# Kernel optimization log

Measured on AMD Instinct MI355X. Metric: run time of the kernel, lower is better.

## Reference

```python
import jax, jax.numpy as jnp
import numpy as np

N_NODES = 100000
N_EDGES = 800000
D_NODE = 64
D_EDGE = 16
D_OUT = 64
D_ATT = 2 * D_OUT + D_EDGE  # 144


def setup_inputs() -> dict:
    key = jax.random.key(0)
    ks = jax.random.split(key, 10)
    node_features = jax.random.normal(ks[0], (N_NODES, D_NODE), dtype=jnp.float32)
    edge_node_indices = jax.random.randint(ks[1], (2, N_EDGES), 0, N_NODES, dtype=jnp.int64)
    edge_features = jax.random.normal(ks[2], (N_EDGES, D_EDGE), dtype=jnp.float32)
    # Linear weights (torch convention: W is [out, in]); uniform(size, w) style init approximated
    def uni(k, shape, size):
        bound = 1.0 / np.sqrt(size)
        return jax.random.uniform(k, shape, dtype=jnp.float32, minval=-bound, maxval=bound)
    W_n = uni(ks[3], (D_OUT, D_NODE), D_NODE)
    b_n = uni(ks[4], (D_OUT,), D_NODE)
    W_e = uni(ks[5], (D_EDGE, D_EDGE), D_EDGE)
    b_e = uni(ks[6], (D_EDGE,), D_EDGE)
    W_a = uni(ks[7], (1, D_ATT), D_ATT)
    b_a = uni(ks[8], (1,), D_ATT)
    return {
        "node_features": node_features,
        "edge_node_indices": edge_node_indices,
        "edge_features": edge_features,
        "W_n": W_n, "b_n": b_n,
        "W_e": W_e, "b_e": b_e,
        "W_a": W_a, "b_a": b_a,
    }


def reference(node_features, edge_node_indices, edge_features, W_n, b_n, W_e, b_e, W_a, b_a):
    node0_idx = edge_node_indices[0]
    node1_idx = edge_node_indices[1]
    n_nodes = node_features.shape[0]

    # gather + linear projections  [E, D_OUT] / [E, D_EDGE]
    node0_out = node_features[node0_idx] @ W_n.T + b_n
    node1_out = node_features[node1_idx] @ W_n.T + b_n
    edge_out = edge_features @ W_e.T + b_e

    # attention over concat -> scalar per edge  [E, 1]
    att_in = jnp.concatenate([node0_out, node1_out, edge_out], axis=1)
    att_out = att_in @ W_a.T + b_a
    # faithful to original: softmax along dim=1 of an [E,1] tensor (== all ones)
    attention = jax.nn.softmax(jax.nn.leaky_relu(att_out, negative_slope=0.01), axis=1)

    # attenuate and scatter-sum back to nodes
    attenuated = attention * node0_out  # [E, D_OUT]
    z = jax.ops.segment_sum(attenuated, node0_idx, num_segments=n_nodes)
    return z
```

## Files before the change

### kernel.cpp

```cpp
#include <hip/hip_runtime.h>
#include <hip/hip_bf16.h>

#define N_NODES 100000
#define N_EDGES 800000
#define D 64
#define SLICES 64
#define QUARTERS 4
#define HIST_BLOCKS (SLICES * QUARTERS)
#define NQUART 25000
#define HWORDS_Q 6272
#define QUADS (N_EDGES / 4)
#define QPS (QUADS / SLICES)
#define XPAD 72

typedef __attribute__((ext_vector_type(8))) short bf16x8;
typedef __attribute__((ext_vector_type(4))) float f32x4;


__global__ __launch_bounds__(1024) void hist_kernel(
        const int* __restrict__ idx32,
        unsigned*  __restrict__ part) {
    __shared__ __align__(16) unsigned h[HWORDS_Q];
    uint4* __restrict__ h4 = (uint4*)h;
    for (int i = threadIdx.x; i < HWORDS_Q / 4; i += 1024)
        h4[i] = uint4{0u, 0u, 0u, 0u};

    const int lane = threadIdx.x & 63;
    int s = 0;
#pragma unroll
    for (int k = 0; k < 4; ++k) s |= idx32[2 * (lane + 64 * k) + 1];
    const bool is64 = (__ballot(s != 0) == 0ULL);

    __syncthreads();

    const int slice = blockIdx.x >> 2;
    const int q     = blockIdx.x & 3;
    const int base  = q * NQUART;

    for (int t = slice * QPS + threadIdx.x; t < (slice + 1) * QPS; t += 1024) {
        int v[4];
        if (is64) {
            const int4 a = ((const int4*)idx32)[2 * t + 0];
            const int4 b = ((const int4*)idx32)[2 * t + 1];
            v[0] = a.x; v[1] = a.z; v[2] = b.x; v[3] = b.z;
        } else {
            const int4 a = ((const int4*)idx32)[t];
            v[0] = a.x; v[1] = a.y; v[2] = a.z; v[3] = a.w;
        }
#pragma unroll
        for (int j = 0; j < 4; ++j) {
            const unsigned u = (unsigned)(v[j] - base);
            if (u < (unsigned)NQUART)
                atomicAdd(&h[u >> 2], 1u << (8 * (u & 3)));
        }
    }

    __syncthreads();

    uint4* __restrict__ dst = (uint4*)(part + (size_t)blockIdx.x * HWORDS_Q);
    for (int i = threadIdx.x; i < HWORDS_Q / 4; i += 1024) dst[i] = h4[i];
}

__device__ inline unsigned bf16rn(float f) {
    const unsigned u = __float_as_uint(f);
    return (u + 0x7FFFu + ((u >> 16) & 1u)) >> 16;
}
__device__ inline unsigned pk2(float lo, float hi) {
    return bf16rn(lo) | (bf16rn(hi) << 16);
}

__global__ __launch_bounds__(256, 4) void proj_kernel(
        const float* __restrict__ nf,
        const float* __restrict__ Wn,
        const float* __restrict__ bn,
        const unsigned* __restrict__ part,
        float* __restrict__ out) {
    __shared__ __align__(16) unsigned short xs[64 * XPAD];
    __shared__ __align__(16) unsigned short wl[64 * XPAD];
    __shared__ unsigned cnt_p[4][64];

    const int t = threadIdx.x;
    const int base = blockIdx.x * 64;
    const int lane = t & 63;
    const int wv = __builtin_amdgcn_readfirstlane(t >> 6);

    {
        const int r = t >> 2;
        const int c0 = (t & 3) * 16;
        const float* __restrict__ src = Wn + r * D + c0;
        const float4 v0 = *reinterpret_cast<const float4*>(src + 0);
        const float4 v1 = *reinterpret_cast<const float4*>(src + 4);
        const float4 v2 = *reinterpret_cast<const float4*>(src + 8);
        const float4 v3 = *reinterpret_cast<const float4*>(src + 12);
        uint4 lo, hi;
        lo.x = pk2(v0.x, v0.y); lo.y = pk2(v0.z, v0.w);
        lo.z = pk2(v1.x, v1.y); lo.w = pk2(v1.z, v1.w);
        hi.x = pk2(v2.x, v2.y); hi.y = pk2(v2.z, v2.w);
        hi.z = pk2(v3.x, v3.y); hi.w = pk2(v3.z, v3.w);
        *reinterpret_cast<uint4*>(&wl[r * XPAD + c0 + 0]) = lo;
        *reinterpret_cast<uint4*>(&wl[r * XPAD + c0 + 8]) = hi;
    }

    {
        const int r = t >> 2;
        const int c0 = (t & 3) * 16;
        const int node = min(base + r, N_NODES - 1);
        const float* __restrict__ src = nf + (size_t)node * D + c0;
        const float4 v0 = *reinterpret_cast<const float4*>(src + 0);
        const float4 v1 = *reinterpret_cast<const float4*>(src + 4);
        const float4 v2 = *reinterpret_cast<const float4*>(src + 8);
        const float4 v3 = *reinterpret_cast<const float4*>(src + 12);
        uint4 lo, hi;
        lo.x = pk2(v0.x, v0.y); lo.y = pk2(v0.z, v0.w);
        lo.z = pk2(v1.x, v1.y); lo.w = pk2(v1.z, v1.w);
        hi.x = pk2(v2.x, v2.y); hi.y = pk2(v2.z, v2.w);
        hi.z = pk2(v3.x, v3.y); hi.w = pk2(v3.z, v3.w);
        *reinterpret_cast<uint4*>(&xs[r * XPAD + c0 + 0]) = lo;
        *reinterpret_cast<uint4*>(&xs[r * XPAD + c0 + 8]) = hi;
    }

    {
        const int node = min(base + lane, N_NODES - 1);
        const int q = node / NQUART;
        const int lw = (node - q * NQUART) >> 2;
        const int sh = 8 * (node & 3);
        unsigned s = 0;
#pragma unroll
        for (int k = 0; k < 16; ++k) {
            const int b = 16 * wv + k;
            s += (part[(size_t)(4 * b + q) * HWORDS_Q + lw] >> sh) & 255u;
        }
        cnt_p[wv][lane] = s;
    }

    __syncthreads();

    const int l15 = lane & 15;
    const int lhi = lane >> 4;

    const unsigned short* __restrict__ arow = &xs[(wv * 16 + l15) * XPAD + lhi * 8];
    const bf16x8 a0 = *reinterpret_cast<const bf16x8*>(arow + 0);
    const bf16x8 a1 = *reinterpret_cast<const bf16x8*>(arow + 32);

    f32x4 acc[4];
#pragma unroll
    for (int nt = 0; nt < 4; ++nt) {
        const float b = bn[nt * 16 + l15];
        acc[nt] = f32x4{b, b, b, b};
    }

#pragma unroll
    for (int nt = 0; nt < 4; ++nt) {
        const unsigned short* __restrict__ brow =
            &wl[(nt * 16 + l15) * XPAD + lhi * 8];
        const bf16x8 b0 = *reinterpret_cast<const bf16x8*>(brow + 0);
        const bf16x8 b1 = *reinterpret_cast<const bf16x8*>(brow + 32);
        acc[nt] = __builtin_amdgcn_mfma_f32_16x16x32_bf16(a0, b0, acc[nt], 0, 0, 0);
        acc[nt] = __builtin_amdgcn_mfma_f32_16x16x32_bf16(a1, b1, acc[nt], 0, 0, 0);
    }

    float cf[4];
#pragma unroll
    for (int r = 0; r < 4; ++r) {
        const int m = wv * 16 + lhi * 4 + r;
        cf[r] = (float)(cnt_p[0][m] + cnt_p[1][m] + cnt_p[2][m] + cnt_p[3][m]);
    }

#pragma unroll
    for (int nt = 0; nt < 4; ++nt) {
#pragma unroll
        for (int r = 0; r < 4; ++r) {
            const int node = base + wv * 16 + lhi * 4 + r;
            if (node < N_NODES)
                out[(size_t)node * D + nt * 16 + l15] = cf[r] * acc[nt][r];
        }
    }
}

extern "C" void kernel_launch(void* const* d_in, const int* in_sizes, int n_in,
                              void* d_out, int out_size, void* d_ws, size_t ws_size,
                              hipStream_t stream) {
    const float* nf   = (const float*)d_in[0];
    const int*   eidx = (const int*)d_in[1];
    const float* Wn   = (const float*)d_in[3];
    const float* bn   = (const float*)d_in[4];
    float* out = (float*)d_out;

    unsigned* part = (unsigned*)d_ws;

    hist_kernel<<<HIST_BLOCKS, 1024, 0, stream>>>(eidx, part);

    proj_kernel<<<(N_NODES + 63) / 64, 256, 0, stream>>>(
        nf, Wn, bn, part, out);
}
```

Before: 24.41 us.

## Fuse histogram and projection into one cooperative kernel with grid sync

Merges the per-node edge-count histogram kernel and the bf16 MFMA projection kernel into a single cooperative launch of 256 blocks of 1024 threads, separated by a grid-wide barrier. The projection phase becomes a persistent loop over 256-node tiles, reusing the converted weight tile and bias across tiles. The aim is to remove the second launch and the gap between kernels. In exchange it adds grid-sync overhead, runs fewer threads in the projection phase than the many small blocks did before, and relies on cooperative launch residency.

Result: slower. 67.65 us (+177.2%).

```diff
diff --git a/kernel.cpp b/kernel.cpp
--- a/kernel.cpp
+++ b/kernel.cpp
@@ -1,65 +1,26 @@
 #include <hip/hip_runtime.h>
 #include <hip/hip_bf16.h>
+#include <hip/hip_cooperative_groups.h>
+
+namespace cg = cooperative_groups;
 
 #define N_NODES 100000
 #define N_EDGES 800000
 #define D 64
 #define SLICES 64
 #define QUARTERS 4
-#define HIST_BLOCKS (SLICES * QUARTERS)
 #define NQUART 25000
 #define HWORDS_Q 6272
 #define QUADS (N_EDGES / 4)
 #define QPS (QUADS / SLICES)
 #define XPAD 72
+#define TILE 256
+#define N_TILES ((N_NODES + TILE - 1) / TILE)
+#define GRID 256
 
 typedef __attribute__((ext_vector_type(8))) short bf16x8;
 typedef __attribute__((ext_vector_type(4))) float f32x4;
 
-
-__global__ __launch_bounds__(1024) void hist_kernel(
-        const int* __restrict__ idx32,
-        unsigned*  __restrict__ part) {
-    __shared__ __align__(16) unsigned h[HWORDS_Q];
-    uint4* __restrict__ h4 = (uint4*)h;
-    for (int i = threadIdx.x; i < HWORDS_Q / 4; i += 1024)
-        h4[i] = uint4{0u, 0u, 0u, 0u};
-
-    const int lane = threadIdx.x & 63;
-    int s = 0;
-#pragma unroll
-    for (int k = 0; k < 4; ++k) s |= idx32[2 * (lane + 64 * k) + 1];
-    const bool is64 = (__ballot(s != 0) == 0ULL);
-
-    __syncthreads();
-
-    const int slice = blockIdx.x >> 2;
-    const int q     = blockIdx.x & 3;
-    const int base  = q * NQUART;
-
-    for (int t = slice * QPS + threadIdx.x; t < (slice + 1) * QPS; t += 1024) {
-        int v[4];
-        if (is64) {
-            const int4 a = ((const int4*)idx32)[2 * t + 0];
-            const int4 b = ((const int4*)idx32)[2 * t + 1];
-            v[0] = a.x; v[1] = a.z; v[2] = b.x; v[3] = b.z;
-        } else {
-            const int4 a = ((const int4*)idx32)[t];
-            v[0] = a.x; v[1] = a.y; v[2] = a.z; v[3] = a.w;
-        }
-#pragma unroll
-        for (int j = 0; j < 4; ++j) {
-            const unsigned u = (unsigned)(v[j] - base);
-            if (u < (unsigned)NQUART)
-                atomicAdd(&h[u >> 2], 1u << (8 * (u & 3)));
-        }
-    }
-
-    __syncthreads();
-
-    uint4* __restrict__ dst = (uint4*)(part + (size_t)blockIdx.x * HWORDS_Q);
-    for (int i = threadIdx.x; i < HWORDS_Q / 4; i += 1024) dst[i] = h4[i];
-}
 
 __device__ inline unsigned bf16rn(float f) {
     const unsigned u = __float_as_uint(f);
@@ -69,22 +30,73 @@
     return bf16rn(lo) | (bf16rn(hi) << 16);
 }
 
-__global__ __launch_bounds__(256, 4) void proj_kernel(
+#define SMEM_BYTES 50176
+
+__global__ __launch_bounds__(1024, 2) void fused_kernel(
+        const int*   __restrict__ idx32,
         const float* __restrict__ nf,
         const float* __restrict__ Wn,
         const float* __restrict__ bn,
-        const unsigned* __restrict__ part,
-        float* __restrict__ out) {
-    __shared__ __align__(16) unsigned short xs[64 * XPAD];
-    __shared__ __align__(16) unsigned short wl[64 * XPAD];
-    __shared__ unsigned cnt_p[4][64];
-
+        unsigned*    __restrict__ part,
+        float*       __restrict__ out) {
+    __shared__ __align__(16) unsigned char smem[SMEM_BYTES];
     const int t = threadIdx.x;
-    const int base = blockIdx.x * 64;
     const int lane = t & 63;
+    cg::grid_group grid = cg::this_grid();
+
+    {
+        unsigned* __restrict__ h = (unsigned*)smem;
+        uint4* __restrict__ h4 = (uint4*)smem;
+        for (int i = t; i < HWORDS_Q / 4; i += 1024)
+            h4[i] = uint4{0u, 0u, 0u, 0u};
+
+        int s = 0;
+#pragma unroll
+        for (int k = 0; k < 4; ++k) s |= idx32[2 * (lane + 64 * k) + 1];
+        const bool is64 = (__ballot(s != 0) == 0ULL);
+
+        __syncthreads();
+
+        const int slice = blockIdx.x >> 2;
+        const int q     = blockIdx.x & 3;
+        const int base  = q * NQUART;
+
+        for (int tq = slice * QPS + t; tq < (slice + 1) * QPS; tq += 1024) {
+            int v[4];
+            if (is64) {
+                const int4 a = ((const int4*)idx32)[2 * tq + 0];
+                const int4 b = ((const int4*)idx32)[2 * tq + 1];
+                v[0] = a.x; v[1] = a.z; v[2] = b.x; v[3] = b.z;
+            } else {
+                const int4 a = ((const int4*)idx32)[tq];
+                v[0] = a.x; v[1] = a.y; v[2] = a.z; v[3] = a.w;
+            }
+#pragma unroll
+            for (int j = 0; j < 4; ++j) {
+                const unsigned u = (unsigned)(v[j] - base);
+                if (u < (unsigned)NQUART)
+                    atomicAdd(&h[u >> 2], 1u << (8 * (u & 3)));
+            }
+        }
+
+        __syncthreads();
+
+        uint4* __restrict__ dst =
+            (uint4*)(part + (size_t)blockIdx.x * HWORDS_Q);
+        for (int i = t; i < HWORDS_Q / 4; i += 1024) dst[i] = h4[i];
+    }
+
+    grid.sync();
+
+    unsigned short* __restrict__ xs = (unsigned short*)smem;
+    unsigned short* __restrict__ wl = (unsigned short*)(smem + 36864);
+    unsigned* __restrict__ cnt_p = (unsigned*)(smem + 36864 + 9216);
+
     const int wv = __builtin_amdgcn_readfirstlane(t >> 6);
-
-    {
+    const int l15 = lane & 15;
+    const int lhi = lane >> 4;
+
+    if (t < 256) {
         const int r = t >> 2;
         const int c0 = (t & 3) * 16;
         const float* __restrict__ src = Wn + r * D + c0;
@@ -101,78 +113,85 @@
         *reinterpret_cast<uint4*>(&wl[r * XPAD + c0 + 8]) = hi;
     }
 
-    {
-        const int r = t >> 2;
-        const int c0 = (t & 3) * 16;
-        const int node = min(base + r, N_NODES - 1);
-        const float* __restrict__ src = nf + (size_t)node * D + c0;
-        const float4 v0 = *reinterpret_cast<const float4*>(src + 0);
-        const float4 v1 = *reinterpret_cast<const float4*>(src + 4);
-        const float4 v2 = *reinterpret_cast<const float4*>(src + 8);
-        const float4 v3 = *reinterpret_cast<const float4*>(src + 12);
-        uint4 lo, hi;
-        lo.x = pk2(v0.x, v0.y); lo.y = pk2(v0.z, v0.w);
-        lo.z = pk2(v1.x, v1.y); lo.w = pk2(v1.z, v1.w);
-        hi.x = pk2(v2.x, v2.y); hi.y = pk2(v2.z, v2.w);
-        hi.z = pk2(v3.x, v3.y); hi.w = pk2(v3.z, v3.w);
-        *reinterpret_cast<uint4*>(&xs[r * XPAD + c0 + 0]) = lo;
-        *reinterpret_cast<uint4*>(&xs[r * XPAD + c0 + 8]) = hi;
-    }
-
-    {
-        const int node = min(base + lane, N_NODES - 1);
-        const int q = node / NQUART;
-        const int lw = (node - q * NQUART) >> 2;
-        const int sh = 8 * (node & 3);
-        unsigned s = 0;
-#pragma unroll
-        for (int k = 0; k < 16; ++k) {
-            const int b = 16 * wv + k;
-            s += (part[(size_t)(4 * b + q) * HWORDS_Q + lw] >> sh) & 255u;
-        }
-        cnt_p[wv][lane] = s;
-    }
-
-    __syncthreads();
-
-    const int l15 = lane & 15;
-    const int lhi = lane >> 4;
-
-    const unsigned short* __restrict__ arow = &xs[(wv * 16 + l15) * XPAD + lhi * 8];
-    const bf16x8 a0 = *reinterpret_cast<const bf16x8*>(arow + 0);
-    const bf16x8 a1 = *reinterpret_cast<const bf16x8*>(arow + 32);
-
-    f32x4 acc[4];
-#pragma unroll
-    for (int nt = 0; nt < 4; ++nt) {
-        const float b = bn[nt * 16 + l15];
-        acc[nt] = f32x4{b, b, b, b};
-    }
-
-#pragma unroll
-    for (int nt = 0; nt < 4; ++nt) {
-        const unsigned short* __restrict__ brow =
-            &wl[(nt * 16 + l15) * XPAD + lhi * 8];
-        const bf16x8 b0 = *reinterpret_cast<const bf16x8*>(brow + 0);
-        const bf16x8 b1 = *reinterpret_cast<const bf16x8*>(brow + 32);
-        acc[nt] = __builtin_amdgcn_mfma_f32_16x16x32_bf16(a0, b0, acc[nt], 0, 0, 0);
-        acc[nt] = __builtin_amdgcn_mfma_f32_16x16x32_bf16(a1, b1, acc[nt], 0, 0, 0);
-    }
-
-    float cf[4];
-#pragma unroll
-    for (int r = 0; r < 4; ++r) {
-        const int m = wv * 16 + lhi * 4 + r;
-        cf[r] = (float)(cnt_p[0][m] + cnt_p[1][m] + cnt_p[2][m] + cnt_p[3][m]);
-    }
-
-#pragma unroll
-    for (int nt = 0; nt < 4; ++nt) {
+    float bias[4];
+#pragma unroll
+    for (int nt = 0; nt < 4; ++nt) bias[nt] = bn[nt * 16 + l15];
+
+    for (int tile = blockIdx.x; tile < N_TILES; tile += GRID) {
+        const int tbase = tile * TILE;
+
+        __syncthreads();
+
+        {
+            const int r = t >> 2;
+            const int c0 = (t & 3) * 16;
+            const int node = min(tbase + r, N_NODES - 1);
+            const float* __restrict__ src = nf + (size_t)node * D + c0;
+            const float4 v0 = *reinterpret_cast<const float4*>(src + 0);
+            const float4 v1 = *reinterpret_cast<const float4*>(src + 4);
+            const float4 v2 = *reinterpret_cast<const float4*>(src + 8);
+            const float4 v3 = *reinterpret_cast<const float4*>(src + 12);
+            uint4 lo, hi;
+            lo.x = pk2(v0.x, v0.y); lo.y = pk2(v0.z, v0.w);
+            lo.z = pk2(v1.x, v1.y); lo.w = pk2(v1.z, v1.w);
+            hi.x = pk2(v2.x, v2.y); hi.y = pk2(v2.z, v2.w);
+            hi.z = pk2(v3.x, v3.y); hi.w = pk2(v3.z, v3.w);
+            *reinterpret_cast<uint4*>(&xs[r * XPAD + c0 + 0]) = lo;
+            *reinterpret_cast<uint4*>(&xs[r * XPAD + c0 + 8]) = hi;
+        }
+
+        {
+            const int node = min(tbase + wv * 16 + l15, N_NODES - 1);
+            const int q = node / NQUART;
+            const int lw = (node - q * NQUART) >> 2;
+            const int sh = 8 * (node & 3);
+            unsigned s = 0;
+#pragma unroll
+            for (int k = 0; k < 16; ++k) {
+                const int b = 16 * lhi + k;
+                s += (part[(size_t)(4 * b + q) * HWORDS_Q + lw] >> sh) & 255u;
+            }
+            cnt_p[wv * 64 + lhi * 16 + l15] = s;
+        }
+
+        __syncthreads();
+
+        const unsigned short* __restrict__ arow =
+            &xs[(wv * 16 + l15) * XPAD + lhi * 8];
+        const bf16x8 a0 = *reinterpret_cast<const bf16x8*>(arow + 0);
+        const bf16x8 a1 = *reinterpret_cast<const bf16x8*>(arow + 32);
+
+        f32x4 acc[4];
+#pragma unroll
+        for (int nt = 0; nt < 4; ++nt)
+            acc[nt] = f32x4{bias[nt], bias[nt], bias[nt], bias[nt]};
+
+#pragma unroll
+        for (int nt = 0; nt < 4; ++nt) {
+            const unsigned short* __restrict__ brow =
+                &wl[(nt * 16 + l15) * XPAD + lhi * 8];
+            const bf16x8 b0 = *reinterpret_cast<const bf16x8*>(brow + 0);
+            const bf16x8 b1 = *reinterpret_cast<const bf16x8*>(brow + 32);
+            acc[nt] = __builtin_amdgcn_mfma_f32_16x16x32_bf16(a0, b0, acc[nt], 0, 0, 0);
+            acc[nt] = __builtin_amdgcn_mfma_f32_16x16x32_bf16(a1, b1, acc[nt], 0, 0, 0);
+        }
+
+        float cf[4];
 #pragma unroll
         for (int r = 0; r < 4; ++r) {
-            const int node = base + wv * 16 + lhi * 4 + r;
-            if (node < N_NODES)
-                out[(size_t)node * D + nt * 16 + l15] = cf[r] * acc[nt][r];
+            const int i = lhi * 4 + r;
+            cf[r] = (float)(cnt_p[wv * 64 + 0 + i] + cnt_p[wv * 64 + 16 + i] +
+                            cnt_p[wv * 64 + 32 + i] + cnt_p[wv * 64 + 48 + i]);
+        }
+
+#pragma unroll
+        for (int nt = 0; nt < 4; ++nt) {
+#pragma unroll
+            for (int r = 0; r < 4; ++r) {
+                const int node = tbase + wv * 16 + lhi * 4 + r;
+                if (node < N_NODES)
+                    out[(size_t)node * D + nt * 16 + l15] = cf[r] * acc[nt][r];
+            }
         }
     }
 }
@@ -180,16 +199,16 @@
 extern "C" void kernel_launch(void* const* d_in, const int* in_sizes, int n_in,
                               void* d_out, int out_size, void* d_ws, size_t ws_size,
                               hipStream_t stream) {
+    const int*   eidx = (const int*)d_in[1];
     const float* nf   = (const float*)d_in[0];
-    const int*   eidx = (const int*)d_in[1];
     const float* Wn   = (const float*)d_in[3];
     const float* bn   = (const float*)d_in[4];
     float* out = (float*)d_out;
 
     unsigned* part = (unsigned*)d_ws;
 
-    hist_kernel<<<HIST_BLOCKS, 1024, 0, stream>>>(eidx, part);
-
-    proj_kernel<<<(N_NODES + 63) / 64, 256, 0, stream>>>(
-        nf, Wn, bn, part, out);
-}
+    void* args[] = {(void*)&eidx, (void*)&nf, (void*)&Wn,
+                    (void*)&bn, (void*)&part, (void*)&out};
+    hipLaunchCooperativeKernel((void*)fused_kernel, dim3(GRID), dim3(1024),
+                               args, 0, stream);
+}
```
